# Kernel tuning notes

Hardware: AMD Instinct MI355X
Metric: run time of the kernel (lower is better)

## Reference

```python
import jax, jax.numpy as jnp
import numpy as np

# Winograd F(4x4, 3x3) transform matrices (wincnn convention, as in jiecaoyu/winograd)
BT = jnp.array([
    [4.,  0., -5.,  0., 1., 0.],
    [0., -4., -4.,  1., 1., 0.],
    [0.,  4., -4., -1., 1., 0.],
    [0., -2., -1.,  2., 1., 0.],
    [0.,  2., -1., -2., 1., 0.],
    [0.,  4.,  0., -5., 0., 1.]], dtype=jnp.float32)  # [6,6]
AT = jnp.array([
    [1., 1.,  1., 1.,  1., 0.],
    [0., 1., -1., 2., -2., 0.],
    [0., 1.,  1., 4.,  4., 0.],
    [0., 1., -1., 8., -8., 1.]], dtype=jnp.float32)  # [4,6]

KERNEL = 3
PAD = 1
GROUPS = 1
TILE_IN = 6   # input_tile_size
TILE_OUT = 4  # output_tile_size


def setup_inputs() -> dict:
    key = jax.random.key(0)
    k1, k2, k3 = jax.random.split(key, 3)
    N, Cin, H, W = 16, 64, 128, 128
    Cout = 64
    x = jax.random.normal(k1, (N, Cin, H, W), dtype=jnp.float32)
    # weight is stored in the Winograd (6x6 spectral) domain, as in the module
    weight = jax.random.normal(k2, (Cout, Cin // GROUPS, TILE_IN, TILE_IN), dtype=jnp.float32) * 0.01
    bias = jax.random.normal(k3, (Cout,), dtype=jnp.float32) * 0.01
    return {"x": x, "weight": weight, "bias": bias}


def reference(x, weight, bias):
    N, Cin, H0, W0 = x.shape
    Cout = weight.shape[0]
    g = GROUPS
    # conv padding
    x = jnp.pad(x, ((0, 0), (0, 0), (PAD, PAD), (PAD, PAD)))
    H = x.shape[2]
    out_w = H - KERNEL + 1
    # pad so output width is a multiple of the output tile size
    extra = (-out_w) % TILE_OUT
    if extra:
        x = jnp.pad(x, ((0, 0), (0, 0), (0, extra), (0, extra)))
    nt = (x.shape[2] - TILE_IN) // TILE_OUT + 1  # tiles per spatial dim
    # extract overlapping 6x6 tiles with stride 4 (the torch unfold)
    idx = jnp.arange(nt)[:, None] * TILE_OUT + jnp.arange(TILE_IN)[None, :]  # [nt,6]
    tiles = x[:, :, idx]                 # [N,C,nt,6,Wp]
    tiles = tiles[:, :, :, :, idx]       # [N,C,nt,6,nt,6]
    # input transform: V = BT @ d @ BT^T per tile -> [N,C,nt,nt,6,6]
    V = jnp.einsum('ai,ncpiqj,bj->ncpqab', BT, tiles, BT)
    # grouped spectral GEMM over input channels
    Vg = V.reshape(N, g, Cin // g, nt, nt, TILE_IN, TILE_IN)
    Wg = weight.reshape(g, Cout // g, Cin // g, TILE_IN, TILE_IN)
    M = jnp.einsum('goiab,ngipqab->ngopqab', Wg, Vg)
    M = M.reshape(N, Cout, nt, nt, TILE_IN, TILE_IN)
    # output transform: Y = AT @ M @ AT^T per tile -> [N,O,nt,nt,4,4]
    Y = jnp.einsum('xa,nopqab,yb->nopqxy', AT, M, AT)
    # stitch tiles back: [N,O,nt,4,nt,4] -> [N,O,nt*4,nt*4]
    y = Y.transpose(0, 1, 2, 4, 3, 5).reshape(N, Cout, nt * TILE_OUT, nt * TILE_OUT)
    y = y + bias[None, :, None, None]
    # crop the extra padding
    y = y[:, :, :out_w, :out_w]
    return y
```

## Files before the change

### kernel.cpp

```cpp
#include <hip/hip_runtime.h>
#include <stdint.h>

typedef __attribute__((ext_vector_type(4))) float f32x4;
typedef __attribute__((ext_vector_type(8))) short s16x8;

#define NTILES_TOTAL 16384
#define WB_BYTES 294912

__device__ __forceinline__ short f2bf(float f) {
    uint32_t u = __builtin_bit_cast(uint32_t, f);
    u = u + 0x7FFFu + ((u >> 16) & 1u);
    return (short)(u >> 16);
}

__global__ __launch_bounds__(256) void wtrans(const float* __restrict__ wf, short* __restrict__ wb) {
    int tid = blockIdx.x * 256 + threadIdx.x;
    const float* src = wf + tid * 36;
    float w[36];
#pragma unroll
    for (int i = 0; i < 9; i++) {
        f32x4 v = *(const f32x4*)(src + 4 * i);
        w[4*i+0] = v[0]; w[4*i+1] = v[1]; w[4*i+2] = v[2]; w[4*i+3] = v[3];
    }
#pragma unroll
    for (int ab = 0; ab < 36; ab++) wb[ab * 4096 + tid] = f2bf(w[ab]);
}

__global__ __launch_bounds__(256) void itrans(const float* __restrict__ x, short* __restrict__ V,
                                              int base_tile) {
    __shared__ float X[144 * 65];
    int t = threadIdx.x;
    int tile0 = base_tile + blockIdx.x * 4;
    int n = tile0 >> 10;
    int rem = tile0 & 1023;
    int p = rem >> 5;
    int q0 = rem & 31;
    const float* xb = x + (size_t)(n * 64) * 16384;
    int row0 = 4 * p - 1;
    int col0 = 4 * q0 - 4;

    for (int s = t; s < 2304; s += 256) {
        int cin = s / 36;
        int rs = s - cin * 36;
        int r = rs / 6;
        int c4 = rs - r * 6;
        int gr = row0 + r;
        int gc = col0 + 4 * c4;
        float v0 = 0.f, v1 = 0.f, v2 = 0.f, v3 = 0.f;
        if ((unsigned)gr < 128u) {
            const float* rowp = xb + (size_t)(cin * 128 + gr) * 128;
            if (gc >= 0 && gc + 3 < 128) {
                f32x4 v = *(const f32x4*)(rowp + gc);
                v0 = v[0]; v1 = v[1]; v2 = v[2]; v3 = v[3];
            } else {
                if ((unsigned)(gc + 0) < 128u) v0 = rowp[gc + 0];
                if ((unsigned)(gc + 1) < 128u) v1 = rowp[gc + 1];
                if ((unsigned)(gc + 2) < 128u) v2 = rowp[gc + 2];
                if ((unsigned)(gc + 3) < 128u) v3 = rowp[gc + 3];
            }
        }
        int b = (r * 24 + 4 * c4) * 65 + cin;
        X[b] = v0; X[b + 65] = v1; X[b + 130] = v2; X[b + 195] = v3;
    }
    __syncthreads();

    int cin = t & 63;
    int ti  = t >> 6;
    int cofs = 4 * ti + 3;
    float U[6][6];
#pragma unroll
    for (int c = 0; c < 6; c++) {
        float m0 = X[(0 * 24 + cofs + c) * 65 + cin];
        float m1 = X[(1 * 24 + cofs + c) * 65 + cin];
        float m2 = X[(2 * 24 + cofs + c) * 65 + cin];
        float m3 = X[(3 * 24 + cofs + c) * 65 + cin];
        float m4 = X[(4 * 24 + cofs + c) * 65 + cin];
        float m5 = X[(5 * 24 + cofs + c) * 65 + cin];
        float g = m4 - m2;
        float e = fmaf(-4.f, m2, m4);
        float f = fmaf(-4.f, m1, m3);
        float h = m3 - m1;
        U[0][c] = fmaf(4.f, m0 - m2, g);
        U[1][c] = e + f;
        U[2][c] = e - f;
        U[3][c] = fmaf(2.f, h, g);
        U[4][c] = fmaf(-2.f, h, g);
        U[5][c] = fmaf(4.f, m1 - m3, m5 - m3);
    }
    int lt = tile0 - base_tile + ti;
    int tg = lt >> 4;
    int t16 = lt & 15;
    short* vb = V + (size_t)tg * 36864 + t16 * 64 + cin;
#pragma unroll
    for (int a = 0; a < 6; a++) {
        float m0 = U[a][0], m1 = U[a][1], m2 = U[a][2], m3 = U[a][3], m4 = U[a][4], m5 = U[a][5];
        float g = m4 - m2;
        float e = fmaf(-4.f, m2, m4);
        float f = fmaf(-4.f, m1, m3);
        float h = m3 - m1;
        vb[(a * 6 + 0) * 1024] = f2bf(fmaf(4.f, m0 - m2, g));
        vb[(a * 6 + 1) * 1024] = f2bf(e + f);
        vb[(a * 6 + 2) * 1024] = f2bf(e - f);
        vb[(a * 6 + 3) * 1024] = f2bf(fmaf(2.f, h, g));
        vb[(a * 6 + 4) * 1024] = f2bf(fmaf(-2.f, h, g));
        vb[(a * 6 + 5) * 1024] = f2bf(fmaf(4.f, m1 - m3, m5 - m3));
    }
}

__global__ __launch_bounds__(256, 2) void wgemm(const short* __restrict__ V, const short* __restrict__ wb,
                                                const float* __restrict__ bias, float* __restrict__ out,
                                                int base_tile) {
    int t = threadIdx.x;
    int lane = t & 63;
    int cog = t >> 6;
    int lo = lane & 15;
    int q = lane >> 4;
    int tg = blockIdx.x;

    const short* wbase = wb + (cog * 16 + lo) * 64 + q * 8;
    const short* vbase = V + (size_t)tg * 36864 + lo * 64 + q * 8;

    f32x4 acc[36];
#pragma unroll
    for (int i = 0; i < 36; i++) acc[i] = (f32x4){0.f, 0.f, 0.f, 0.f};

#pragma unroll
    for (int ab = 0; ab < 36; ab++) {
        s16x8 a0 = *(const s16x8*)(wbase + ab * 4096);
        s16x8 a1 = *(const s16x8*)(wbase + ab * 4096 + 32);
        s16x8 b0 = *(const s16x8*)(vbase + ab * 1024);
        s16x8 b1 = *(const s16x8*)(vbase + ab * 1024 + 32);
        acc[ab] = __builtin_amdgcn_mfma_f32_16x16x32_bf16(a0, b0, acc[ab], 0, 0, 0);
        acc[ab] = __builtin_amdgcn_mfma_f32_16x16x32_bf16(a1, b1, acc[ab], 0, 0, 0);
    }

    int gt = base_tile + tg * 16 + lo;
    int n = gt >> 10;
    int remt = gt & 1023;
    int p = remt >> 5;
    int qq = remt & 31;
#pragma unroll
    for (int r = 0; r < 4; r++) {
        int co = cog * 16 + q * 4 + r;
        float bv = bias[co];
        float z[4][6];
#pragma unroll
        for (int b = 0; b < 6; b++) {
            float m0 = acc[0 * 6 + b][r], m1 = acc[1 * 6 + b][r], m2 = acc[2 * 6 + b][r];
            float m3 = acc[3 * 6 + b][r], m4 = acc[4 * 6 + b][r], m5 = acc[5 * 6 + b][r];
            float s = m1 + m2, d = m1 - m2, s2 = m3 + m4, d2 = m3 - m4;
            z[0][b] = m0 + s + s2;
            z[1][b] = fmaf(2.f, d2, d);
            z[2][b] = fmaf(4.f, s2, s);
            z[3][b] = fmaf(8.f, d2, d) + m5;
        }
        float* ob = out + ((size_t)(n * 64 + co) * 128 + 4 * p) * 128 + 4 * qq;
#pragma unroll
        for (int xr = 0; xr < 4; xr++) {
            float s = z[xr][1] + z[xr][2], d = z[xr][1] - z[xr][2];
            float s2 = z[xr][3] + z[xr][4], d2 = z[xr][3] - z[xr][4];
            f32x4 y;
            y[0] = z[xr][0] + s + s2 + bv;
            y[1] = fmaf(2.f, d2, d) + bv;
            y[2] = fmaf(4.f, s2, s) + bv;
            y[3] = fmaf(8.f, d2, d) + z[xr][5] + bv;
            *(f32x4*)(ob + xr * 128) = y;
        }
    }
}

extern "C" void kernel_launch(void* const* d_in, const int* in_sizes, int n_in,
                              void* d_out, int out_size, void* d_ws, size_t ws_size,
                              hipStream_t stream) {
    const float* x    = (const float*)d_in[0];
    const float* wf   = (const float*)d_in[1];
    const float* bias = (const float*)d_in[2];
    float* out = (float*)d_out;

    short* wb = (short*)d_ws;
    short* V  = (short*)((char*)d_ws + WB_BYTES);

    const size_t v_full = 75497472ull;
    int chunks = 0;
    const int cand[5] = {1, 2, 4, 8, 16};
    for (int i = 0; i < 5; i++) {
        if ((size_t)WB_BYTES + v_full / (size_t)cand[i] <= ws_size) { chunks = cand[i]; break; }
    }
    if (!chunks) return;

    wtrans<<<16, 256, 0, stream>>>(wf, wb);
    int tiles_per_chunk = NTILES_TOTAL / chunks;
    for (int i = 0; i < chunks; i++) {
        int base = i * tiles_per_chunk;
        itrans<<<tiles_per_chunk / 4, 256, 0, stream>>>(x, V, base);
        wgemm<<<tiles_per_chunk / 16, 256, 0, stream>>>(V, wb, bias, out, base);
    }
}
```

Measured before the change: 210.3 us.

## Stage V tiles in LDS via global_load_lds with XOR swizzle in wgemm

In the spectral GEMM, the block's V slice is now loaded into shared memory with direct global-to-LDS async loads, in two halves of 18 spectral positions each. Fragments are then read from LDS using an XOR swizzle to avoid bank conflicts. Previously each of the four waves loaded the same V data straight from global memory. The aim is to share the V loads across the four output-channel groups and cut redundant global and L2 traffic. In exchange it uses 36 KB of LDS per block and adds barriers, which may limit occupancy and serialise loads with compute.

Result: faster. 186.8 us (-11.2%).

```diff
diff --git a/kernel.cpp b/kernel.cpp
--- a/kernel.cpp
+++ b/kernel.cpp
@@ -3,6 +3,9 @@
 
 typedef __attribute__((ext_vector_type(4))) float f32x4;
 typedef __attribute__((ext_vector_type(8))) short s16x8;
+
+typedef __attribute__((address_space(1))) const char g8_t;
+typedef __attribute__((address_space(3))) char lds8_t;
 
 #define NTILES_TOTAL 16384
 #define WB_BYTES 294912
@@ -110,28 +113,48 @@
 __global__ __launch_bounds__(256, 2) void wgemm(const short* __restrict__ V, const short* __restrict__ wb,
                                                 const float* __restrict__ bias, float* __restrict__ out,
                                                 int base_tile) {
+    __shared__ __align__(16) short Vs[18432];
     int t = threadIdx.x;
     int lane = t & 63;
     int cog = t >> 6;
     int lo = lane & 15;
-    int q = lane >> 4;
+    int kq = lane >> 4;
     int tg = blockIdx.x;
 
-    const short* wbase = wb + (cog * 16 + lo) * 64 + q * 8;
-    const short* vbase = V + (size_t)tg * 36864 + lo * 64 + q * 8;
+    const char* vtg = (const char*)V + (size_t)tg * 73728;
+    const short* wbase = wb + (cog * 16 + lo) * 64 + kq * 8;
 
     f32x4 acc[36];
 #pragma unroll
     for (int i = 0; i < 36; i++) acc[i] = (f32x4){0.f, 0.f, 0.f, 0.f};
 
-#pragma unroll
-    for (int ab = 0; ab < 36; ab++) {
-        s16x8 a0 = *(const s16x8*)(wbase + ab * 4096);
-        s16x8 a1 = *(const s16x8*)(wbase + ab * 4096 + 32);
-        s16x8 b0 = *(const s16x8*)(vbase + ab * 1024);
-        s16x8 b1 = *(const s16x8*)(vbase + ab * 1024 + 32);
-        acc[ab] = __builtin_amdgcn_mfma_f32_16x16x32_bf16(a0, b0, acc[ab], 0, 0, 0);
-        acc[ab] = __builtin_amdgcn_mfma_f32_16x16x32_bf16(a1, b1, acc[ab], 0, 0, 0);
+    int xs = (lo & 7);
+
+#pragma unroll
+    for (int rnd = 0; rnd < 2; rnd++) {
+        const char* src0 = vtg + rnd * 36864;
+#pragma unroll
+        for (int i = 0; i < 9; i++) {
+            int chunk = i * 256 + t;
+            int row = (chunk >> 3) & 15;
+            int csw = (chunk & ~7) | ((chunk ^ row) & 7);
+            lds8_t* ldst = (lds8_t*)Vs + (i * 256 + (t & ~63)) * 16;
+            __builtin_amdgcn_global_load_lds((g8_t*)(src0 + csw * 16), ldst, 16, 0, 0);
+        }
+        __syncthreads();
+
+#pragma unroll
+        for (int abl = 0; abl < 18; abl++) {
+            int ab = rnd * 18 + abl;
+            s16x8 a0 = *(const s16x8*)(wbase + ab * 4096);
+            s16x8 a1 = *(const s16x8*)(wbase + ab * 4096 + 32);
+            const short* vrow = Vs + abl * 1024 + lo * 64;
+            s16x8 b0 = *(const s16x8*)(vrow + ((kq ^ xs) << 3));
+            s16x8 b1 = *(const s16x8*)(vrow + (((4 + kq) ^ xs) << 3));
+            acc[ab] = __builtin_amdgcn_mfma_f32_16x16x32_bf16(a0, b0, acc[ab], 0, 0, 0);
+            acc[ab] = __builtin_amdgcn_mfma_f32_16x16x32_bf16(a1, b1, acc[ab], 0, 0, 0);
+        }
+        if (rnd == 0) __syncthreads();
     }
 
     int gt = base_tile + tg * 16 + lo;
@@ -141,7 +164,7 @@
     int qq = remt & 31;
 #pragma unroll
     for (int r = 0; r < 4; r++) {
-        int co = cog * 16 + q * 4 + r;
+        int co = cog * 16 + kq * 4 + r;
         float bv = bias[co];
         float z[4][6];
 #pragma unroll
```

## Fuse Winograd input transform and spectral GEMM into one kernel

Applied to the files above, without the earlier changes.

Replaces the separate input-transform and GEMM kernels with a single fused kernel. Each block loads an 18x18 halo patch for a 4x4 group of tiles in two 32-channel halves, transforms them in LDS, and feeds MFMA directly, so the bf16 V tensor never goes through global memory and the chunked workspace logic is removed. The cost is more syncthreads per block, larger LDS use that may limit occupancy, and weights reloaded from global per block.

Measured after the change: 180.7 us. 1.16x faster.

```diff
diff --git a/kernel.cpp b/kernel.cpp
--- a/kernel.cpp
+++ b/kernel.cpp
@@ -4,7 +4,6 @@
 typedef __attribute__((ext_vector_type(4))) float f32x4;
 typedef __attribute__((ext_vector_type(8))) short s16x8;
 
-#define NTILES_TOTAL 16384
 #define WB_BYTES 294912
 
 __device__ __forceinline__ short f2bf(float f) {
@@ -26,144 +25,154 @@
     for (int ab = 0; ab < 36; ab++) wb[ab * 4096 + tid] = f2bf(w[ab]);
 }
 
-__global__ __launch_bounds__(256) void itrans(const float* __restrict__ x, short* __restrict__ V,
-                                              int base_tile) {
-    __shared__ float X[144 * 65];
-    int t = threadIdx.x;
-    int tile0 = base_tile + blockIdx.x * 4;
-    int n = tile0 >> 10;
-    int rem = tile0 & 1023;
-    int p = rem >> 5;
-    int q0 = rem & 31;
-    const float* xb = x + (size_t)(n * 64) * 16384;
-    int row0 = 4 * p - 1;
-    int col0 = 4 * q0 - 4;
-
-    for (int s = t; s < 2304; s += 256) {
-        int cin = s / 36;
-        int rs = s - cin * 36;
-        int r = rs / 6;
-        int c4 = rs - r * 6;
-        int gr = row0 + r;
-        int gc = col0 + 4 * c4;
-        float v0 = 0.f, v1 = 0.f, v2 = 0.f, v3 = 0.f;
-        if ((unsigned)gr < 128u) {
-            const float* rowp = xb + (size_t)(cin * 128 + gr) * 128;
-            if (gc >= 0 && gc + 3 < 128) {
-                f32x4 v = *(const f32x4*)(rowp + gc);
-                v0 = v[0]; v1 = v[1]; v2 = v[2]; v3 = v[3];
-            } else {
-                if ((unsigned)(gc + 0) < 128u) v0 = rowp[gc + 0];
-                if ((unsigned)(gc + 1) < 128u) v1 = rowp[gc + 1];
-                if ((unsigned)(gc + 2) < 128u) v2 = rowp[gc + 2];
-                if ((unsigned)(gc + 3) < 128u) v3 = rowp[gc + 3];
-            }
-        }
-        int b = (r * 24 + 4 * c4) * 65 + cin;
-        X[b] = v0; X[b + 65] = v1; X[b + 130] = v2; X[b + 195] = v3;
-    }
-    __syncthreads();
-
-    int cin = t & 63;
-    int ti  = t >> 6;
-    int cofs = 4 * ti + 3;
-    float U[6][6];
-#pragma unroll
-    for (int c = 0; c < 6; c++) {
-        float m0 = X[(0 * 24 + cofs + c) * 65 + cin];
-        float m1 = X[(1 * 24 + cofs + c) * 65 + cin];
-        float m2 = X[(2 * 24 + cofs + c) * 65 + cin];
-        float m3 = X[(3 * 24 + cofs + c) * 65 + cin];
-        float m4 = X[(4 * 24 + cofs + c) * 65 + cin];
-        float m5 = X[(5 * 24 + cofs + c) * 65 + cin];
-        float g = m4 - m2;
-        float e = fmaf(-4.f, m2, m4);
-        float f = fmaf(-4.f, m1, m3);
-        float h = m3 - m1;
-        U[0][c] = fmaf(4.f, m0 - m2, g);
-        U[1][c] = e + f;
-        U[2][c] = e - f;
-        U[3][c] = fmaf(2.f, h, g);
-        U[4][c] = fmaf(-2.f, h, g);
-        U[5][c] = fmaf(4.f, m1 - m3, m5 - m3);
-    }
-    int lt = tile0 - base_tile + ti;
-    int tg = lt >> 4;
-    int t16 = lt & 15;
-    short* vb = V + (size_t)tg * 36864 + t16 * 64 + cin;
-#pragma unroll
-    for (int a = 0; a < 6; a++) {
-        float m0 = U[a][0], m1 = U[a][1], m2 = U[a][2], m3 = U[a][3], m4 = U[a][4], m5 = U[a][5];
-        float g = m4 - m2;
-        float e = fmaf(-4.f, m2, m4);
-        float f = fmaf(-4.f, m1, m3);
-        float h = m3 - m1;
-        vb[(a * 6 + 0) * 1024] = f2bf(fmaf(4.f, m0 - m2, g));
-        vb[(a * 6 + 1) * 1024] = f2bf(e + f);
-        vb[(a * 6 + 2) * 1024] = f2bf(e - f);
-        vb[(a * 6 + 3) * 1024] = f2bf(fmaf(2.f, h, g));
-        vb[(a * 6 + 4) * 1024] = f2bf(fmaf(-2.f, h, g));
-        vb[(a * 6 + 5) * 1024] = f2bf(fmaf(4.f, m1 - m3, m5 - m3));
-    }
-}
-
-__global__ __launch_bounds__(256, 2) void wgemm(const short* __restrict__ V, const short* __restrict__ wb,
-                                                const float* __restrict__ bias, float* __restrict__ out,
-                                                int base_tile) {
+#define XS 343
+__global__ __launch_bounds__(256, 2) void wino_fused(const float* __restrict__ x,
+                                                     const short* __restrict__ wb,
+                                                     const float* __restrict__ bias,
+                                                     float* __restrict__ out) {
+    __shared__ float X[32 * XS];
+    __shared__ __align__(16) short Vs[18 * 16 * 32];
     int t = threadIdx.x;
     int lane = t & 63;
     int cog = t >> 6;
     int lo = lane & 15;
-    int q = lane >> 4;
-    int tg = blockIdx.x;
+    int kq = lane >> 4;
 
-    const short* wbase = wb + (cog * 16 + lo) * 64 + q * 8;
-    const short* vbase = V + (size_t)tg * 36864 + lo * 64 + q * 8;
+    int b = blockIdx.x;
+    int n = b >> 6;
+    int sb = b & 63;
+    int p0 = (sb >> 3) * 4;
+    int q0 = (sb & 7) * 4;
+    const float* xb = x + (size_t)n * 64 * 16384;
+    int row0 = 4 * p0 - 1;
+    int col0a = 4 * q0 - 4;
+
+    int cin = t & 31;
+    int tl0 = t >> 5;
 
     f32x4 acc[36];
 #pragma unroll
     for (int i = 0; i < 36; i++) acc[i] = (f32x4){0.f, 0.f, 0.f, 0.f};
 
 #pragma unroll
-    for (int ab = 0; ab < 36; ab++) {
-        s16x8 a0 = *(const s16x8*)(wbase + ab * 4096);
-        s16x8 a1 = *(const s16x8*)(wbase + ab * 4096 + 32);
-        s16x8 b0 = *(const s16x8*)(vbase + ab * 1024);
-        s16x8 b1 = *(const s16x8*)(vbase + ab * 1024 + 32);
-        acc[ab] = __builtin_amdgcn_mfma_f32_16x16x32_bf16(a0, b0, acc[ab], 0, 0, 0);
-        acc[ab] = __builtin_amdgcn_mfma_f32_16x16x32_bf16(a1, b1, acc[ab], 0, 0, 0);
+    for (int r = 0; r < 2; r++) {
+#pragma unroll
+        for (int i = 0; i < 14; i++) {
+            int s = i * 256 + t;
+            if (s < 3456) {
+                int ci = s / 108;
+                int rs = s - ci * 108;
+                int row = rs / 6;
+                int c4 = rs - row * 6;
+                int gr = row0 + row;
+                int gc = col0a + 4 * c4;
+                float v0 = 0.f, v1 = 0.f, v2 = 0.f, v3 = 0.f;
+                if ((unsigned)gr < 128u) {
+                    const float* rowp = xb + (size_t)((r * 32 + ci) * 128 + gr) * 128;
+                    if (gc >= 0 && gc + 3 < 128) {
+                        f32x4 v = *(const f32x4*)(rowp + gc);
+                        v0 = v[0]; v1 = v[1]; v2 = v[2]; v3 = v[3];
+                    } else {
+                        if ((unsigned)(gc + 0) < 128u) v0 = rowp[gc + 0];
+                        if ((unsigned)(gc + 1) < 128u) v1 = rowp[gc + 1];
+                        if ((unsigned)(gc + 2) < 128u) v2 = rowp[gc + 2];
+                        if ((unsigned)(gc + 3) < 128u) v3 = rowp[gc + 3];
+                    }
+                }
+                int base = ci * XS + row * 18;
+                int cl = 4 * c4 - 3;
+                if ((unsigned)(cl + 0) < 18u) X[base + cl + 0] = v0;
+                if ((unsigned)(cl + 1) < 18u) X[base + cl + 1] = v1;
+                if ((unsigned)(cl + 2) < 18u) X[base + cl + 2] = v2;
+                if ((unsigned)(cl + 3) < 18u) X[base + cl + 3] = v3;
+            }
+        }
+        __syncthreads();
+
+#pragma unroll
+        for (int s = 0; s < 2; s++) {
+#pragma unroll
+            for (int task = 0; task < 2; task++) {
+                int tl = tl0 + task * 8;
+                int tp = tl >> 2, tq = tl & 3;
+                const float* Xb = X + cin * XS + (4 * tp) * 18 + 4 * tq;
+                float Ua[3][6];
+#pragma unroll
+                for (int c = 0; c < 6; c++) {
+                    float m0 = Xb[0 * 18 + c], m1 = Xb[1 * 18 + c], m2 = Xb[2 * 18 + c];
+                    float m3 = Xb[3 * 18 + c], m4 = Xb[4 * 18 + c], m5 = Xb[5 * 18 + c];
+                    if (s == 0) {
+                        float e = fmaf(-4.f, m2, m4);
+                        float f = fmaf(-4.f, m1, m3);
+                        Ua[0][c] = fmaf(4.f, m0 - m2, m4 - m2);
+                        Ua[1][c] = e + f;
+                        Ua[2][c] = e - f;
+                    } else {
+                        float g = m4 - m2;
+                        float h = m3 - m1;
+                        Ua[0][c] = fmaf(2.f, h, g);
+                        Ua[1][c] = fmaf(-2.f, h, g);
+                        Ua[2][c] = fmaf(4.f, m1 - m3, m5 - m3);
+                    }
+                }
+                short* vb = Vs + tl * 32 + cin;
+#pragma unroll
+                for (int ar = 0; ar < 3; ar++) {
+                    float m0 = Ua[ar][0], m1 = Ua[ar][1], m2 = Ua[ar][2];
+                    float m3 = Ua[ar][3], m4 = Ua[ar][4], m5 = Ua[ar][5];
+                    float e = fmaf(-4.f, m2, m4);
+                    float f = fmaf(-4.f, m1, m3);
+                    float g = m4 - m2;
+                    float h = m3 - m1;
+                    vb[(ar * 6 + 0) * 512] = f2bf(fmaf(4.f, m0 - m2, g));
+                    vb[(ar * 6 + 1) * 512] = f2bf(e + f);
+                    vb[(ar * 6 + 2) * 512] = f2bf(e - f);
+                    vb[(ar * 6 + 3) * 512] = f2bf(fmaf(2.f, h, g));
+                    vb[(ar * 6 + 4) * 512] = f2bf(fmaf(-2.f, h, g));
+                    vb[(ar * 6 + 5) * 512] = f2bf(fmaf(4.f, m1 - m3, m5 - m3));
+                }
+            }
+            __syncthreads();
+
+            const short* wb_base = wb + (s * 18) * 4096 + (cog * 16 + lo) * 64 + r * 32 + kq * 8;
+            const short* v_base = Vs + lo * 32 + kq * 8;
+#pragma unroll
+            for (int abl = 0; abl < 18; abl++) {
+                s16x8 a0 = *(const s16x8*)(wb_base + abl * 4096);
+                s16x8 b0 = *(const s16x8*)(v_base + abl * 512);
+                acc[s * 18 + abl] = __builtin_amdgcn_mfma_f32_16x16x32_bf16(a0, b0, acc[s * 18 + abl], 0, 0, 0);
+            }
+            __syncthreads();
+        }
     }
 
-    int gt = base_tile + tg * 16 + lo;
-    int n = gt >> 10;
-    int remt = gt & 1023;
-    int p = remt >> 5;
-    int qq = remt & 31;
+    int p = p0 + (lo >> 2);
+    int q = q0 + (lo & 3);
 #pragma unroll
-    for (int r = 0; r < 4; r++) {
-        int co = cog * 16 + q * 4 + r;
+    for (int rr = 0; rr < 4; rr++) {
+        int co = cog * 16 + kq * 4 + rr;
         float bv = bias[co];
         float z[4][6];
 #pragma unroll
-        for (int b = 0; b < 6; b++) {
-            float m0 = acc[0 * 6 + b][r], m1 = acc[1 * 6 + b][r], m2 = acc[2 * 6 + b][r];
-            float m3 = acc[3 * 6 + b][r], m4 = acc[4 * 6 + b][r], m5 = acc[5 * 6 + b][r];
-            float s = m1 + m2, d = m1 - m2, s2 = m3 + m4, d2 = m3 - m4;
-            z[0][b] = m0 + s + s2;
-            z[1][b] = fmaf(2.f, d2, d);
-            z[2][b] = fmaf(4.f, s2, s);
-            z[3][b] = fmaf(8.f, d2, d) + m5;
+        for (int bb = 0; bb < 6; bb++) {
+            float m0 = acc[0 * 6 + bb][rr], m1 = acc[1 * 6 + bb][rr], m2 = acc[2 * 6 + bb][rr];
+            float m3 = acc[3 * 6 + bb][rr], m4 = acc[4 * 6 + bb][rr], m5 = acc[5 * 6 + bb][rr];
+            float s1 = m1 + m2, d1 = m1 - m2, s2 = m3 + m4, d2 = m3 - m4;
+            z[0][bb] = m0 + s1 + s2;
+            z[1][bb] = fmaf(2.f, d2, d1);
+            z[2][bb] = fmaf(4.f, s2, s1);
+            z[3][bb] = fmaf(8.f, d2, d1) + m5;
         }
-        float* ob = out + ((size_t)(n * 64 + co) * 128 + 4 * p) * 128 + 4 * qq;
+        float* ob = out + ((size_t)(n * 64 + co) * 128 + 4 * p) * 128 + 4 * q;
 #pragma unroll
         for (int xr = 0; xr < 4; xr++) {
-            float s = z[xr][1] + z[xr][2], d = z[xr][1] - z[xr][2];
+            float s1 = z[xr][1] + z[xr][2], d1 = z[xr][1] - z[xr][2];
             float s2 = z[xr][3] + z[xr][4], d2 = z[xr][3] - z[xr][4];
             f32x4 y;
-            y[0] = z[xr][0] + s + s2 + bv;
-            y[1] = fmaf(2.f, d2, d) + bv;
-            y[2] = fmaf(4.f, s2, s) + bv;
-            y[3] = fmaf(8.f, d2, d) + z[xr][5] + bv;
+            y[0] = z[xr][0] + s1 + s2 + bv;
+            y[1] = fmaf(2.f, d2, d1) + bv;
+            y[2] = fmaf(4.f, s2, s1) + bv;
+            y[3] = fmaf(8.f, d2, d1) + z[xr][5] + bv;
             *(f32x4*)(ob + xr * 128) = y;
         }
     }
@@ -177,22 +186,9 @@
     const float* bias = (const float*)d_in[2];
     float* out = (float*)d_out;
 
+    if (ws_size < WB_BYTES) return;
     short* wb = (short*)d_ws;
-    short* V  = (short*)((char*)d_ws + WB_BYTES);
-
-    const size_t v_full = 75497472ull;
-    int chunks = 0;
-    const int cand[5] = {1, 2, 4, 8, 16};
-    for (int i = 0; i < 5; i++) {
-        if ((size_t)WB_BYTES + v_full / (size_t)cand[i] <= ws_size) { chunks = cand[i]; break; }
-    }
-    if (!chunks) return;
 
     wtrans<<<16, 256, 0, stream>>>(wf, wb);
-    int tiles_per_chunk = NTILES_TOTAL / chunks;
-    for (int i = 0; i < chunks; i++) {
-        int base = i * tiles_per_chunk;
-        itrans<<<tiles_per_chunk / 4, 256, 0, stream>>>(x, V, base);
-        wgemm<<<tiles_per_chunk / 16, 256, 0, stream>>>(V, wb, bias, out, base);
-    }
+    wino_fused<<<1024, 256, 0, stream>>>(x, wb, bias, out);
 }
```
